# Performance work log

Hardware: AMD Instinct MI355X
Metric: run time of the kernel (lower is better)

## Reference

```python
import jax, jax.numpy as jnp
import numpy as np

N = 100000
D = 128
E = 1600000
L = 3
LN_EPS = 1e-5
SM_EPS = 1e-16  # PyG softmax denominator eps
NEG_SLOPE = 0.2  # GATConv leaky_relu slope


def setup_inputs() -> dict:
    key = jax.random.key(0)
    ks = jax.random.split(key, 9)
    x = jax.random.normal(ks[0], (N, D), dtype=jnp.float32)
    edge_index = jax.random.randint(ks[1], (2, E), 0, N, dtype=jnp.int64)
    # Per-level GATConv params (heads=1, concat -> out dim D)
    W = jax.random.normal(ks[2], (L, D, D), dtype=jnp.float32) / np.sqrt(D)
    att_src = jax.random.normal(ks[3], (L, D), dtype=jnp.float32) / np.sqrt(D)
    att_dst = jax.random.normal(ks[4], (L, D), dtype=jnp.float32) / np.sqrt(D)
    bias = jnp.zeros((L, D), dtype=jnp.float32)
    ln_gamma = jnp.ones((L, D), dtype=jnp.float32)
    ln_beta = jnp.zeros((L, D), dtype=jnp.float32)
    return {"x": x, "edge_index": edge_index, "W": W, "att_src": att_src,
            "att_dst": att_dst, "bias": bias, "ln_gamma": ln_gamma, "ln_beta": ln_beta}


def _gat_level(x, src, dst, W, a_src, a_dst, b):
    h = x @ W                                   # [N, D] transformed features
    alpha_s = h @ a_src                         # [N] per-node src attention logit
    alpha_d = h @ a_dst                         # [N]
    alpha = alpha_s[src] + alpha_d[dst]         # [E'] edge logits
    alpha = jax.nn.leaky_relu(alpha, NEG_SLOPE)
    amax = jax.ops.segment_max(alpha, dst, num_segments=N)  # self-loops guarantee nonempty segments
    alpha = jnp.exp(alpha - amax[dst])
    denom = jax.ops.segment_sum(alpha, dst, num_segments=N)
    alpha = alpha / (denom[dst] + SM_EPS)       # segment softmax over incoming edges
    msg = h[src] * alpha[:, None]               # [E', D]
    out = jax.ops.segment_sum(msg, dst, num_segments=N)
    return out + b


def reference(x, edge_index, W, att_src, att_dst, bias, ln_gamma, ln_beta):
    loops = jnp.arange(N, dtype=edge_index.dtype)
    src = jnp.concatenate([edge_index[0], loops])  # PyG GATConv adds self-loops
    dst = jnp.concatenate([edge_index[1], loops])
    for i in range(L):
        x_att = _gat_level(x, src, dst, W[i], att_src[i], att_dst[i], bias[i])
        y = x + x_att
        mu = jnp.mean(y, axis=-1, keepdims=True)
        var = jnp.mean(jnp.square(y - mu), axis=-1, keepdims=True)
        y = (y - mu) * jax.lax.rsqrt(var + LN_EPS) * ln_gamma[i] + ln_beta[i]
        x = jax.nn.relu(y)  # dropout is identity in eval mode
    return x
```

## Files before the change

### kernel.cpp

```cpp
#include <hip/hip_runtime.h>
#include <hip/hip_fp16.h>
#include <cstdint>

#define D 128
#define NEG_SLOPE 0.2f
#define LN_EPS 1e-5f
#define SM_EPS 1e-16f

typedef _Float16 f16x8 __attribute__((ext_vector_type(8)));
typedef float f32x4 __attribute__((ext_vector_type(4)));


__global__ void hist_dst(const int* __restrict__ dst, int E,
                         int* __restrict__ deg, int* __restrict__ rank) {
    int e = blockIdx.x * blockDim.x + threadIdx.x;
    if (e < E) rank[e] = atomicAdd(&deg[dst[e]], 1);
}

__global__ void scanA(const int* __restrict__ deg, int n,
                      int* __restrict__ excl, int* __restrict__ bsums) {
    __shared__ int s[256];
    int t = threadIdx.x;
    int v = blockIdx.x * 256 + t;
    int d = (v < n) ? deg[v] : 0;
    s[t] = d;
    __syncthreads();
    for (int off = 1; off < 256; off <<= 1) {
        int tv = (t >= off) ? s[t - off] : 0;
        __syncthreads();
        s[t] += tv;
        __syncthreads();
    }
    if (v < n) excl[v] = s[t] - d;
    if (t == 255) bsums[blockIdx.x] = s[255];
}

__global__ void scanB(int* __restrict__ bsums, int nb) {
    __shared__ int s[512];
    int t = threadIdx.x;
    int v = (t < nb) ? bsums[t] : 0;
    s[t] = v;
    __syncthreads();
    for (int off = 1; off < 512; off <<= 1) {
        int tv = (t >= off) ? s[t - off] : 0;
        __syncthreads();
        s[t] += tv;
        __syncthreads();
    }
    if (t < nb) bsums[t] = s[t] - v;
}

__global__ void scanC(int* __restrict__ rowptr, const int* __restrict__ bsums,
                      int n, int total) {
    int v = blockIdx.x * blockDim.x + threadIdx.x;
    if (v < n) rowptr[v] += bsums[v >> 8];
    if (v == 0) rowptr[n] = total;
}

__global__ void fill_csr(const int* __restrict__ src, const int* __restrict__ dst,
                         const int* __restrict__ rank, int E,
                         const int* __restrict__ rowptr, int* __restrict__ col) {
    int e = blockIdx.x * blockDim.x + threadIdx.x;
    if (e >= E) return;
    int d = dst[e];
    int p = rowptr[d] + rank[e];
    atomicExch(&col[p], src[e]);
}


__global__ void prep_w(const float* __restrict__ W, const float* __restrict__ a_src,
                       const float* __restrict__ a_dst, __half* __restrict__ Wt,
                       float* __restrict__ wsv, float* __restrict__ wdv) {
    int l = blockIdx.x >> 3;
    int part = blockIdx.x & 7;
    const float* Wl = W + (size_t)l * D * D;
    __half* Wtl = Wt + (size_t)l * D * D;
    int t = threadIdx.x;
    int c0 = part * 16;

    __shared__ float sT[128][17];
    #pragma unroll
    for (int i = 0; i < 8; ++i) {
        int id = i * 256 + t;
        int k = id >> 4, c = id & 15;
        sT[k][c] = Wl[(size_t)k * D + c0 + c];
    }
    __syncthreads();
    {
        int c = t >> 4, kg = t & 15;
        union { __half hv[8]; float4 f4; } u;
        #pragma unroll
        for (int j = 0; j < 8; ++j) u.hv[j] = __float2half(sT[kg * 8 + j][c]);
        *(float4*)(Wtl + (size_t)(c0 + c) * D + kg * 8) = u.f4;
    }

    if (part == 0) {
        __shared__ float sA[D], sD[D];
        if (t < D) { sA[t] = a_src[l * D + t]; sD[t] = a_dst[l * D + t]; }
        __syncthreads();
        if (t < D) {
            float ps = 0.f, pd = 0.f;
            for (int c = 0; c < D; ++c) {
                float wv = Wl[(size_t)t * D + c];
                ps += wv * sA[c];
                pd += wv * sD[c];
            }
            wsv[l * D + t] = ps;
            wdv[l * D + t] = pd;
        }
    }
}


__global__ __launch_bounds__(256) void gemm_mfma(
        const float* __restrict__ x, const __half* __restrict__ Wt,
        const float* __restrict__ wsv, const float* __restrict__ wdv,
        __half* __restrict__ h, float* __restrict__ as_, float* __restrict__ ad_, int n) {
    __shared__ char sXa[32768];
    __shared__ char sWb[32768];
    int t = threadIdx.x;
    int row0 = blockIdx.x * 128;
    int lane = t & 63;
    int w = t >> 6;
    int wrow = (w >> 1) * 64;
    int wcol = (w & 1) * 64;

    const float4* xv = (const float4*)x;
    #pragma unroll
    for (int i = 0; i < 16; ++i) {
        int slot = i * 256 + t;
        int r = slot >> 5;
        int c4 = slot & 31;
        int gr = row0 + r;
        float4 v = (gr < n) ? xv[(size_t)gr * 32 + c4] : make_float4(0.f, 0.f, 0.f, 0.f);
        union { __half2 q[2]; float2 f; } u;
        u.q[0] = __floats2half2_rn(v.x, v.y);
        u.q[1] = __floats2half2_rn(v.z, v.w);
        *(float2*)(sXa + r * 256 + ((c4 * 8) ^ ((r & 7) << 4))) = u.f;
    }
    const float4* wv = (const float4*)Wt;
    #pragma unroll
    for (int i = 0; i < 8; ++i) {
        int chunk = i * 256 + t;
        int r = chunk >> 4;
        int c16 = chunk & 15;
        float4 v = wv[chunk];
        *(float4*)(sWb + r * 256 + ((c16 * 16) ^ ((r & 7) << 4))) = v;
    }
    __syncthreads();

    f32x4 acc[4][4];
    #pragma unroll
    for (int a = 0; a < 4; ++a)
        #pragma unroll
        for (int b = 0; b < 4; ++b) acc[a][b] = (f32x4){0.f, 0.f, 0.f, 0.f};

    #pragma unroll
    for (int ks = 0; ks < 4; ++ks) {
        int kbyte = ks * 64 + (lane >> 4) * 16;
        f16x8 aF[4], bF[4];
        #pragma unroll
        for (int tt = 0; tt < 4; ++tt) {
            int ra = wrow + tt * 16 + (lane & 15);
            aF[tt] = *(f16x8*)(sXa + ra * 256 + (kbyte ^ ((ra & 7) << 4)));
            int rb = wcol + tt * 16 + (lane & 15);
            bF[tt] = *(f16x8*)(sWb + rb * 256 + (kbyte ^ ((rb & 7) << 4)));
        }
        #pragma unroll
        for (int tr = 0; tr < 4; ++tr)
            #pragma unroll
            for (int tc = 0; tc < 4; ++tc)
                acc[tr][tc] = __builtin_amdgcn_mfma_f32_16x16x32_f16(aF[tr], bF[tc], acc[tr][tc], 0, 0, 0);
    }

    {
        int r = t >> 1, hh = t & 1;
        float ps = 0.f, pd = 0.f;
        const float4* s4 = (const float4*)wsv + hh * 16;
        const float4* d4 = (const float4*)wdv + hh * 16;
        #pragma unroll
        for (int g = 0; g < 8; ++g) {
            int kbyte = hh * 128 + g * 16;
            f16x8 xa = *(f16x8*)(sXa + r * 256 + (kbyte ^ ((r & 7) << 4)));
            float4 sa = s4[g * 2], sb = s4[g * 2 + 1];
            float4 da = d4[g * 2], db = d4[g * 2 + 1];
            ps += (float)xa[0] * sa.x + (float)xa[1] * sa.y + (float)xa[2] * sa.z + (float)xa[3] * sa.w
                + (float)xa[4] * sb.x + (float)xa[5] * sb.y + (float)xa[6] * sb.z + (float)xa[7] * sb.w;
            pd += (float)xa[0] * da.x + (float)xa[1] * da.y + (float)xa[2] * da.z + (float)xa[3] * da.w
                + (float)xa[4] * db.x + (float)xa[5] * db.y + (float)xa[6] * db.z + (float)xa[7] * db.w;
        }
        ps += __shfl_xor(ps, 1);
        pd += __shfl_xor(pd, 1);
        if (hh == 0 && row0 + r < n) { as_[row0 + r] = ps; ad_[row0 + r] = pd; }
    }

    __syncthreads();
    #pragma unroll
    for (int tr = 0; tr < 4; ++tr) {
        int rloc = wrow + tr * 16 + (lane >> 4) * 4;
        #pragma unroll
        for (int reg = 0; reg < 4; ++reg) {
            int r = rloc + reg;
            int swz = (r & 7) << 4;
            #pragma unroll
            for (int tc = 0; tc < 4; ++tc) {
                int c = wcol + tc * 16 + (lane & 15);
                *(__half*)(sWb + r * 256 + ((c * 2) ^ swz)) = __float2half(acc[tr][tc][reg]);
            }
        }
    }
    __syncthreads();
    {
        int r = t >> 1;
        int gr = row0 + r;
        if (gr < n) {
            int halfsel = (t & 1) * 128;
            int swz = (r & 7) << 4;
            #pragma unroll
            for (int j = 0; j < 8; ++j) {
                float4 v = *(float4*)(sWb + r * 256 + ((halfsel + j * 16) ^ swz));
                *(float4*)(h + (size_t)gr * D + (t & 1) * 64 + j * 8) = v;
            }
        }
    }
}


__global__ __launch_bounds__(256) void aggregate(
        const float* __restrict__ xin, const __half* __restrict__ h,
        const float* __restrict__ as_, const float* __restrict__ ad_,
        const int* __restrict__ col, const int* __restrict__ rowptr,
        const float* __restrict__ bias, const float* __restrict__ gamma,
        const float* __restrict__ beta, float* __restrict__ xout, int n) {
    __shared__ int2 sSW[4][64];
    int tid = threadIdx.x;
    int wslot = tid >> 6;
    int lane = tid & 63;
    int wid = (int)((blockIdx.x * blockDim.x + tid) >> 6);
    if (wid >= n) return;
    int v = wid;
    int grp = lane >> 4;
    int gl  = lane & 15;
    int start = rowptr[v], end = rowptr[v + 1];
    float adv = ad_[v];
    float self_a = as_[v] + adv;
    self_a = (self_a > 0.f) ? self_a : NEG_SLOPE * self_a;

    float mval = self_a;
    int   s0r = 0;
    float a0r = -1e30f;
    for (int cb = start; cb < end; cb += 64) {
        int e = cb + lane;
        int   sl = 0;
        float al = -1e30f;
        if (e < end) {
            sl = col[e];
            float aa = as_[sl] + adv;
            al = (aa > 0.f) ? aa : NEG_SLOPE * aa;
        }
        if (cb == start) { s0r = sl; a0r = al; }
        mval = fmaxf(mval, al);
    }
    #pragma unroll
    for (int d = 32; d >= 1; d >>= 1) mval = fmaxf(mval, __shfl_xor(mval, d));

    float wl = __expf(a0r - mval);
    float sacc = wl;
    {
        __half2 wp = __float2half2_rn(wl);
        sSW[wslot][lane] = make_int2(s0r, *(int*)&wp);
    }

    __half2 hacc[4];
    #pragma unroll
    for (int j = 0; j < 4; ++j) hacc[j] = __float2half2_rn(0.f);

    const float4* h4 = (const float4*)h;

    for (int cb = start; cb < end; cb += 64) {
        if (cb != start) {
            int e = cb + lane;
            int   sl = 0;
            float al = -1e30f;
            if (e < end) {
                sl = col[e];
                float aa = as_[sl] + adv;
                al = (aa > 0.f) ? aa : NEG_SLOPE * aa;
            }
            float wl2 = __expf(al - mval);
            sacc += wl2;
            __half2 wp = __float2half2_rn(wl2);
            sSW[wslot][lane] = make_int2(sl, *(int*)&wp);
        }
        int cnt = min(64, end - cb);
        int i = grp;
        if (i < cnt) {
            int2 e0 = sSW[wslot][i];
            float4 u0 = h4[(size_t)e0.x * 16 + gl];
            for (i += 4; i < cnt; i += 4) {
                int2 e1 = sSW[wslot][i];
                float4 u1 = h4[(size_t)e1.x * 16 + gl];
                __half2 w2 = *(__half2*)&e0.y;
                union { float4 f4; __half2 h2[4]; } u;
                u.f4 = u0;
                #pragma unroll
                for (int j = 0; j < 4; ++j) hacc[j] = __hfma2(u.h2[j], w2, hacc[j]);
                e0 = e1; u0 = u1;
            }
            __half2 w2 = *(__half2*)&e0.y;
            union { float4 f4; __half2 h2[4]; } u;
            u.f4 = u0;
            #pragma unroll
            for (int j = 0; j < 4; ++j) hacc[j] = __hfma2(u.h2[j], w2, hacc[j]);
        }
    }
    #pragma unroll
    for (int d = 32; d >= 1; d >>= 1) sacc += __shfl_xor(sacc, d);

    float acc[8];
    #pragma unroll
    for (int j = 0; j < 4; ++j) {
        float2 f = __half22float2(hacc[j]);
        acc[2 * j] = f.x;
        acc[2 * j + 1] = f.y;
    }
    #pragma unroll
    for (int j = 0; j < 8; ++j) {
        acc[j] += __shfl_xor(acc[j], 16);
        acc[j] += __shfl_xor(acc[j], 32);
    }

    float w_self = __expf(self_a - mval);
    sacc += w_self;
    {
        union { float4 f4; __half2 h2[4]; } u;
        u.f4 = h4[(size_t)v * 16 + gl];
        #pragma unroll
        for (int j = 0; j < 4; ++j) {
            float2 f = __half22float2(u.h2[j]);
            acc[2 * j]     += w_self * f.x;
            acc[2 * j + 1] += w_self * f.y;
        }
    }
    float inv = 1.f / (sacc + SM_EPS);

    const float4* xr = (const float4*)(xin + (size_t)v * D) + gl * 2;
    float4 xa = xr[0], xb = xr[1];
    const float4* b4 = (const float4*)bias + gl * 2;
    float4 ba = b4[0], bb = b4[1];
    float y[8];
    y[0] = xa.x + acc[0] * inv + ba.x;
    y[1] = xa.y + acc[1] * inv + ba.y;
    y[2] = xa.z + acc[2] * inv + ba.z;
    y[3] = xa.w + acc[3] * inv + ba.w;
    y[4] = xb.x + acc[4] * inv + bb.x;
    y[5] = xb.y + acc[5] * inv + bb.y;
    y[6] = xb.z + acc[6] * inv + bb.z;
    y[7] = xb.w + acc[7] * inv + bb.w;

    float s2 = 0.f;
    #pragma unroll
    for (int j = 0; j < 8; ++j) s2 += y[j];
    #pragma unroll
    for (int d = 8; d >= 1; d >>= 1) s2 += __shfl_xor(s2, d);
    float mu = s2 * (1.f / 128.f);
    float vs = 0.f;
    #pragma unroll
    for (int j = 0; j < 8; ++j) { float dd = y[j] - mu; vs += dd * dd; }
    #pragma unroll
    for (int d = 8; d >= 1; d >>= 1) vs += __shfl_xor(vs, d);
    float rstd = rsqrtf(vs * (1.f / 128.f) + LN_EPS);

    const float4* g4 = (const float4*)gamma + gl * 2;
    const float4* t4 = (const float4*)beta + gl * 2;
    float4 ga = g4[0], gb = g4[1];
    float4 ta = t4[0], tb = t4[1];
    float4 oa, ob;
    oa.x = fmaxf((y[0] - mu) * rstd * ga.x + ta.x, 0.f);
    oa.y = fmaxf((y[1] - mu) * rstd * ga.y + ta.y, 0.f);
    oa.z = fmaxf((y[2] - mu) * rstd * ga.z + ta.z, 0.f);
    oa.w = fmaxf((y[3] - mu) * rstd * ga.w + ta.w, 0.f);
    ob.x = fmaxf((y[4] - mu) * rstd * gb.x + tb.x, 0.f);
    ob.y = fmaxf((y[5] - mu) * rstd * gb.y + tb.y, 0.f);
    ob.z = fmaxf((y[6] - mu) * rstd * gb.z + tb.z, 0.f);
    ob.w = fmaxf((y[7] - mu) * rstd * gb.w + tb.w, 0.f);

    if (lane < 16) {
        float4* o4 = (float4*)(xout + (size_t)v * D) + gl * 2;
        o4[0] = oa;
        o4[1] = ob;
    }
}


extern "C" void kernel_launch(void* const* d_in, const int* in_sizes, int n_in,
                              void* d_out, int out_size, void* d_ws, size_t ws_size,
                              hipStream_t stream) {
    const float* x       = (const float*)d_in[0];
    const int*   edge    = (const int*)d_in[1];
    const float* W       = (const float*)d_in[2];
    const float* att_src = (const float*)d_in[3];
    const float* att_dst = (const float*)d_in[4];
    const float* bias    = (const float*)d_in[5];
    const float* gamma   = (const float*)d_in[6];
    const float* beta    = (const float*)d_in[7];
    float* out = (float*)d_out;

    const int N = in_sizes[0] / D;
    const int E = in_sizes[1] / 2;

    const int* src = edge;
    const int* dst = edge + E;

    char* ws = (char*)d_ws;
    size_t off = 0;
    auto carve = [&](size_t bytes) -> char* {
        char* p = ws + off;
        off = (off + bytes + 511) & ~(size_t)511;
        return p;
    };
    int*    rowptr = (int*)carve((size_t)(N + 1) * 4);
    int*    deg    = (int*)carve((size_t)N * 4);
    int*    bsums  = (int*)carve(512 * 4);
    int*    col    = (int*)carve((size_t)E * 4);
    int*    rank   = (int*)carve((size_t)E * 4);
    __half* h      = (__half*)carve((size_t)N * D * 2);
    float*  as_    = (float*)carve((size_t)N * 4);
    float*  ad_    = (float*)carve((size_t)N * 4);
    float*  x1     = (float*)carve((size_t)N * D * 4);
    __half* Wt     = (__half*)carve((size_t)3 * D * D * 2);
    float*  wsv    = (float*)carve((size_t)3 * D * 4);
    float*  wdv    = (float*)carve((size_t)3 * D * 4);
    (void)ws_size;

    const int TPB = 256;
    int nbN = (N + TPB - 1) / TPB;
    int nbE = (E + TPB - 1) / TPB;

    prep_w<<<24, TPB, 0, stream>>>(W, att_src, att_dst, Wt, wsv, wdv);

    hipMemsetAsync(deg, 0, (size_t)N * 4, stream);
    hist_dst<<<nbE, TPB, 0, stream>>>(dst, E, deg, rank);
    scanA<<<nbN, TPB, 0, stream>>>(deg, N, rowptr, bsums);
    scanB<<<1, 512, 0, stream>>>(bsums, nbN);
    scanC<<<nbN, TPB, 0, stream>>>(rowptr, bsums, N, E);
    fill_csr<<<nbE, TPB, 0, stream>>>(src, dst, rank, E, rowptr, col);

    int gemmGrid = (N + 127) / 128;
    int aggGrid  = (N * 64 + TPB - 1) / TPB;

    const float* xin = x;
    float* bufs[3] = { x1, x1, out };
    for (int l = 0; l < 3; ++l) {
        const __half* Wtl = Wt + (size_t)l * D * D;
        const float*  wsl = wsv + (size_t)l * D;
        const float*  wdl = wdv + (size_t)l * D;
        const float*  bl  = bias + (size_t)l * D;
        const float*  gl  = gamma + (size_t)l * D;
        const float*  btl = beta + (size_t)l * D;
        float* xout = bufs[l];

        gemm_mfma<<<gemmGrid, TPB, 0, stream>>>(xin, Wtl, wsl, wdl, h, as_, ad_, N);
        aggregate<<<aggGrid, TPB, 0, stream>>>(xin, h, as_, ad_, col, rowptr,
                                               bl, gl, btl, xout, N);
        xin = xout;
    }
}
```

Baseline: 588.2 us.

## Load X fragments directly from global into registers in GEMM, drop X LDS tile

The GEMM kernel no longer stages the 128-row X tile in shared memory. Each wave now owns 32 rows across all 128 columns and loads its A fragments straight from global memory, converting to fp16 in registers, while W stays in LDS. The attention logit dot products are computed in fp32 from the same registers and reduced with lane shuffles, and the output staging swizzle is changed to match the new row layout. This halves LDS use (better occupancy) and removes a barrier and an LDS round trip, at the cost of less coalesced, strided 32-byte global reads of X.

```diff
diff --git a/kernel.cpp b/kernel.cpp
--- a/kernel.cpp
+++ b/kernel.cpp
@@ -116,28 +116,15 @@
         const float* __restrict__ x, const __half* __restrict__ Wt,
         const float* __restrict__ wsv, const float* __restrict__ wdv,
         __half* __restrict__ h, float* __restrict__ as_, float* __restrict__ ad_, int n) {
-    __shared__ char sXa[32768];
     __shared__ char sWb[32768];
     int t = threadIdx.x;
-    int row0 = blockIdx.x * 128;
     int lane = t & 63;
     int w = t >> 6;
-    int wrow = (w >> 1) * 64;
-    int wcol = (w & 1) * 64;
-
-    const float4* xv = (const float4*)x;
-    #pragma unroll
-    for (int i = 0; i < 16; ++i) {
-        int slot = i * 256 + t;
-        int r = slot >> 5;
-        int c4 = slot & 31;
-        int gr = row0 + r;
-        float4 v = (gr < n) ? xv[(size_t)gr * 32 + c4] : make_float4(0.f, 0.f, 0.f, 0.f);
-        union { __half2 q[2]; float2 f; } u;
-        u.q[0] = __floats2half2_rn(v.x, v.y);
-        u.q[1] = __floats2half2_rn(v.z, v.w);
-        *(float2*)(sXa + r * 256 + ((c4 * 8) ^ ((r & 7) << 4))) = u.f;
-    }
+    int rowB = blockIdx.x * 128;
+    int row0 = rowB + w * 32;
+    int rl = lane & 15;
+    int kg = lane >> 4;
+
     const float4* wv = (const float4*)Wt;
     #pragma unroll
     for (int i = 0; i < 8; ++i) {
@@ -149,76 +136,99 @@
     }
     __syncthreads();
 
-    f32x4 acc[4][4];
-    #pragma unroll
-    for (int a = 0; a < 4; ++a)
-        #pragma unroll
-        for (int b = 0; b < 4; ++b) acc[a][b] = (f32x4){0.f, 0.f, 0.f, 0.f};
+    f32x4 acc[2][8];
+    #pragma unroll
+    for (int a = 0; a < 2; ++a)
+        #pragma unroll
+        for (int b = 0; b < 8; ++b) acc[a][b] = (f32x4){0.f, 0.f, 0.f, 0.f};
+    float dsv[2] = {0.f, 0.f}, ddv[2] = {0.f, 0.f};
 
     #pragma unroll
     for (int ks = 0; ks < 4; ++ks) {
-        int kbyte = ks * 64 + (lane >> 4) * 16;
-        f16x8 aF[4], bF[4];
-        #pragma unroll
-        for (int tt = 0; tt < 4; ++tt) {
-            int ra = wrow + tt * 16 + (lane & 15);
-            aF[tt] = *(f16x8*)(sXa + ra * 256 + (kbyte ^ ((ra & 7) << 4)));
-            int rb = wcol + tt * 16 + (lane & 15);
-            bF[tt] = *(f16x8*)(sWb + rb * 256 + (kbyte ^ ((rb & 7) << 4)));
-        }
-        #pragma unroll
-        for (int tr = 0; tr < 4; ++tr)
+        int kf = ks * 32 + kg * 8;
+        int kbyte = ks * 64 + kg * 16;
+
+        f16x8 bF[8];
+        #pragma unroll
+        for (int tc = 0; tc < 8; ++tc) {
+            int rb = tc * 16 + rl;
+            bF[tc] = *(f16x8*)(sWb + rb * 256 + (kbyte ^ ((rb & 7) << 4)));
+        }
+
+        float4 wsa = *(const float4*)(wsv + kf);
+        float4 wsb = *(const float4*)(wsv + kf + 4);
+        float4 wda = *(const float4*)(wdv + kf);
+        float4 wdb = *(const float4*)(wdv + kf + 4);
+
+        f16x8 aF[2];
+        #pragma unroll
+        for (int tt = 0; tt < 2; ++tt) {
+            int gr = row0 + tt * 16 + rl;
+            float4 va = make_float4(0.f, 0.f, 0.f, 0.f);
+            float4 vb = va;
+            if (gr < n) {
+                const float* xr = x + (size_t)gr * D + kf;
+                va = *(const float4*)xr;
+                vb = *(const float4*)(xr + 4);
+            }
+            union { __half2 q[4]; f16x8 f; } u;
+            u.q[0] = __floats2half2_rn(va.x, va.y);
+            u.q[1] = __floats2half2_rn(va.z, va.w);
+            u.q[2] = __floats2half2_rn(vb.x, vb.y);
+            u.q[3] = __floats2half2_rn(vb.z, vb.w);
+            aF[tt] = u.f;
+            dsv[tt] += va.x * wsa.x + va.y * wsa.y + va.z * wsa.z + va.w * wsa.w
+                     + vb.x * wsb.x + vb.y * wsb.y + vb.z * wsb.z + vb.w * wsb.w;
+            ddv[tt] += va.x * wda.x + va.y * wda.y + va.z * wda.z + va.w * wda.w
+                     + vb.x * wdb.x + vb.y * wdb.y + vb.z * wdb.z + vb.w * wdb.w;
+        }
+
+        #pragma unroll
+        for (int tt = 0; tt < 2; ++tt)
             #pragma unroll
-            for (int tc = 0; tc < 4; ++tc)
-                acc[tr][tc] = __builtin_amdgcn_mfma_f32_16x16x32_f16(aF[tr], bF[tc], acc[tr][tc], 0, 0, 0);
-    }
-
-    {
-        int r = t >> 1, hh = t & 1;
-        float ps = 0.f, pd = 0.f;
-        const float4* s4 = (const float4*)wsv + hh * 16;
-        const float4* d4 = (const float4*)wdv + hh * 16;
-        #pragma unroll
-        for (int g = 0; g < 8; ++g) {
-            int kbyte = hh * 128 + g * 16;
-            f16x8 xa = *(f16x8*)(sXa + r * 256 + (kbyte ^ ((r & 7) << 4)));
-            float4 sa = s4[g * 2], sb = s4[g * 2 + 1];
-            float4 da = d4[g * 2], db = d4[g * 2 + 1];
-            ps += (float)xa[0] * sa.x + (float)xa[1] * sa.y + (float)xa[2] * sa.z + (float)xa[3] * sa.w
-                + (float)xa[4] * sb.x + (float)xa[5] * sb.y + (float)xa[6] * sb.z + (float)xa[7] * sb.w;
-            pd += (float)xa[0] * da.x + (float)xa[1] * da.y + (float)xa[2] * da.z + (float)xa[3] * da.w
-                + (float)xa[4] * db.x + (float)xa[5] * db.y + (float)xa[6] * db.z + (float)xa[7] * db.w;
-        }
-        ps += __shfl_xor(ps, 1);
-        pd += __shfl_xor(pd, 1);
-        if (hh == 0 && row0 + r < n) { as_[row0 + r] = ps; ad_[row0 + r] = pd; }
-    }
-
-    __syncthreads();
-    #pragma unroll
-    for (int tr = 0; tr < 4; ++tr) {
-        int rloc = wrow + tr * 16 + (lane >> 4) * 4;
+            for (int tc = 0; tc < 8; ++tc)
+                acc[tt][tc] = __builtin_amdgcn_mfma_f32_16x16x32_f16(aF[tt], bF[tc], acc[tt][tc], 0, 0, 0);
+    }
+
+    #pragma unroll
+    for (int tt = 0; tt < 2; ++tt) {
+        dsv[tt] += __shfl_xor(dsv[tt], 16);
+        dsv[tt] += __shfl_xor(dsv[tt], 32);
+        ddv[tt] += __shfl_xor(ddv[tt], 16);
+        ddv[tt] += __shfl_xor(ddv[tt], 32);
+    }
+    if (lane < 16) {
+        #pragma unroll
+        for (int tt = 0; tt < 2; ++tt) {
+            int gr = row0 + tt * 16 + lane;
+            if (gr < n) { as_[gr] = dsv[tt]; ad_[gr] = ddv[tt]; }
+        }
+    }
+
+    __syncthreads();
+    #pragma unroll
+    for (int tt = 0; tt < 2; ++tt) {
         #pragma unroll
         for (int reg = 0; reg < 4; ++reg) {
-            int r = rloc + reg;
-            int swz = (r & 7) << 4;
+            int rloc = w * 32 + tt * 16 + kg * 4 + reg;
+            int swz = ((rloc >> 2) & 3) << 5;
             #pragma unroll
-            for (int tc = 0; tc < 4; ++tc) {
-                int c = wcol + tc * 16 + (lane & 15);
-                *(__half*)(sWb + r * 256 + ((c * 2) ^ swz)) = __float2half(acc[tr][tc][reg]);
+            for (int tc = 0; tc < 8; ++tc) {
+                int c = tc * 16 + rl;
+                *(__half*)(sWb + rloc * 256 + ((c * 2) ^ swz)) = __float2half(acc[tt][tc][reg]);
             }
         }
     }
     __syncthreads();
     {
         int r = t >> 1;
-        int gr = row0 + r;
+        int gr = rowB + r;
         if (gr < n) {
-            int halfsel = (t & 1) * 128;
-            int swz = (r & 7) << 4;
+            int halfs = (t & 1) * 128;
+            int swz = ((r >> 2) & 3) << 5;
             #pragma unroll
             for (int j = 0; j < 8; ++j) {
-                float4 v = *(float4*)(sWb + r * 256 + ((halfsel + j * 16) ^ swz));
+                float4 v = *(float4*)(sWb + r * 256 + ((halfs + j * 16) ^ swz));
                 *(float4*)(h + (size_t)gr * D + (t & 1) * 64 + j * 8) = v;
             }
         }
```

Result: no change. 580.6 us (-1.3%).
